# Kernel tuning notes

Measured on AMD Instinct MI355X. Metric: run time of the kernel, lower is better.

Reference implementation:

```python
import jax, jax.numpy as jnp
import numpy as np

NUM_HEADS = 8
EPS = 1e-3

N_TOKENS = 32768
DIM = 256
N_WIN = 128
WIN = N_TOKENS // N_WIN  # 256 tokens per window


def setup_inputs() -> dict:
    key = jax.random.key(0)
    ks = jax.random.split(key, 4)
    x = jax.random.normal(ks[0], (N_TOKENS, DIM), dtype=jnp.float32)
    # torch nn.Linear weights are [out_features, in_features]
    w_qkv = jax.random.normal(ks[1], (3 * DIM, DIM), dtype=jnp.float32) * (DIM ** -0.5)
    w_proj = jax.random.normal(ks[2], (DIM, DIM), dtype=jnp.float32) * (DIM ** -0.5)
    b_proj = jnp.zeros((DIM,), dtype=jnp.float32)
    batch_win_inds = (jnp.arange(N_TOKENS) // WIN).astype(jnp.int64)
    offsets = (jnp.arange(N_WIN) * WIN).astype(jnp.int64)
    counts = jnp.full((N_WIN,), WIN, dtype=jnp.int64)
    return {"x": x, "w_qkv": w_qkv, "w_proj": w_proj, "b_proj": b_proj,
            "offsets": offsets, "counts": counts, "batch_win_inds": batch_win_inds}


def reference(x, w_qkv, w_proj, b_proj, offsets, counts, batch_win_inds):
    N, C = x.shape
    H = NUM_HEADS
    hd = C // H
    W = counts.shape[0]  # number of windows (static)

    qkv = x @ w_qkv.T                      # [N, 3C]
    q, k, v = jnp.split(qkv, 3, axis=-1)   # each [N, C]
    q = jax.nn.relu(q.reshape(N, H, hd))   # [N, H, hd]
    k = jax.nn.relu(k.reshape(N, H, hd))
    v = v.reshape(N, H, hd)

    seg = batch_win_inds.astype(jnp.int32)
    # per-window KV state: kv[w] = sum_{i in w} k_i^T v_i   -> [W, H, hd, hd]
    kv = jax.ops.segment_sum(jnp.einsum('nhc,nhd->nhcd', k, v), seg, num_segments=W)
    # per-window key sum for normalizer                      -> [W, H, hd]
    s = jax.ops.segment_sum(k, seg, num_segments=W)

    y = jnp.einsum('nhc,nhcd->nhd', q, kv[seg])              # [N, H, hd]
    z = jnp.sum(s[seg] * q, axis=-1, keepdims=True)          # [N, H, 1]
    y = y / (z + EPS)

    y = y.reshape(N, C) @ w_proj.T + b_proj                  # [N, C]
    return y
```

## Files before the change

### kernel.cpp

```cpp
#include <hip/hip_runtime.h>

typedef __bf16 bf16_t;
typedef bf16_t bf16x8 __attribute__((ext_vector_type(8)));
typedef bf16_t bf16x4 __attribute__((ext_vector_type(4)));
typedef float f32x4 __attribute__((ext_vector_type(4)));

#define M_TOK 32768
#define NWIN 128
#define WIN  256

typedef __attribute__((address_space(3))) void* as3p;
typedef const __attribute__((address_space(1))) void* as1p;

__device__ __forceinline__ void gll16(const void* g, void* l) {
    __builtin_amdgcn_global_load_lds((as1p)g, (as3p)l, 16, 0, 0);
}

__device__ __forceinline__ bf16x8 cvt8(f32x4 a, f32x4 b) {
    bf16x8 o;
    o[0] = (bf16_t)a[0]; o[1] = (bf16_t)a[1]; o[2] = (bf16_t)a[2]; o[3] = (bf16_t)a[3];
    o[4] = (bf16_t)b[0]; o[5] = (bf16_t)b[1]; o[6] = (bf16_t)b[2]; o[7] = (bf16_t)b[3];
    return o;
}

__global__ __launch_bounds__(256) void wconv(
    const float* __restrict__ wq, const float* __restrict__ wp,
    bf16_t* __restrict__ wqb, bf16_t* __restrict__ wpb)
{
    int i4 = (blockIdx.x * 256 + threadIdx.x) * 4;
    const float* s; bf16_t* dst; int idx;
    if (i4 < 196608) { s = wq; dst = wqb; idx = i4; }
    else             { s = wp; dst = wpb; idx = i4 - 196608; }
    f32x4 v = *(const f32x4*)(s + idx);
    bf16x4 o;
    o[0] = (bf16_t)v[0]; o[1] = (bf16_t)v[1]; o[2] = (bf16_t)v[2]; o[3] = (bf16_t)v[3];
    *(bf16x4*)(dst + idx) = o;
}

__global__ __launch_bounds__(256) void gemm1_qkv(
    const float* __restrict__ X,
    const bf16_t* __restrict__ Wb,
    bf16_t* __restrict__ QKV)
{
    __shared__ float  As[4][128][16];
    __shared__ bf16_t Bs[2][128][32];

    const int tid = threadIdx.x;
    const int lane = tid & 63;
    const int wv = tid >> 6;
    const int wm = wv >> 1, wn = wv & 1;
    const int id = blockIdx.x;
    const int sg = id / 48, wsub = id % 48;
    const int m0 = (sg * 8 + (wsub & 7)) * 128;
    const int n0 = (wsub >> 3) * 128;
    const int r = lane & 15, q = lane >> 4;
    const int srow = lane >> 2;

    f32x4 acc[4][4] = {};

    for (int kc = 0; kc < 256; kc += 64) {
#pragma unroll
        for (int p = 0; p < 4; ++p)
#pragma unroll
            for (int g = 0; g < 2; ++g) {
                const int rb = wv * 32 + g * 16;
                gll16(X + (size_t)(m0 + rb + srow) * 256 + kc + p * 16 + (lane & 3) * 4,
                      &As[p][rb][0]);
            }
#pragma unroll
        for (int p = 0; p < 2; ++p)
#pragma unroll
            for (int g = 0; g < 2; ++g) {
                const int rb = wv * 32 + g * 16;
                gll16(Wb + (size_t)(n0 + rb + srow) * 256 + kc + p * 32 + (lane & 3) * 8,
                      &Bs[p][rb][0]);
            }
        __syncthreads();

#pragma unroll
        for (int kk = 0; kk < 64; kk += 32) {
            const int kq = kk + q * 8;
            const int pA = kq >> 4, offA = kq & 15;
            const int pB = kk >> 5;
            bf16x8 a[4], b[4];
#pragma unroll
            for (int i = 0; i < 4; ++i) {
                f32x4 lo = *(const f32x4*)&As[pA][wm * 64 + i * 16 + r][offA];
                f32x4 hi = *(const f32x4*)&As[pA][wm * 64 + i * 16 + r][offA + 4];
                a[i] = cvt8(lo, hi);
            }
#pragma unroll
            for (int j = 0; j < 4; ++j)
                b[j] = *(const bf16x8*)&Bs[pB][wn * 64 + j * 16 + r][q * 8];
#pragma unroll
            for (int i = 0; i < 4; ++i)
#pragma unroll
                for (int j = 0; j < 4; ++j)
                    acc[i][j] = __builtin_amdgcn_mfma_f32_16x16x32_bf16(b[j], a[i], acc[i][j], 0, 0, 0);
        }
        __syncthreads();
    }

#pragma unroll
    for (int i = 0; i < 4; ++i) {
        const int rowg = m0 + wm * 64 + i * 16 + r;
#pragma unroll
        for (int j = 0; j < 4; ++j) {
            const int nb = n0 + wn * 64 + j * 16 + q * 4;
            const int nblk = nb >> 5, d = nb & 31;
            bf16x4 o;
#pragma unroll
            for (int reg = 0; reg < 4; ++reg) {
                float v = acc[i][j][reg];
                if (nblk < 16) v = fmaxf(v, 0.0f);
                o[reg] = (bf16_t)v;
            }
            *(bf16x4*)&QKV[((size_t)nblk * M_TOK + rowg) * 32 + d] = o;
        }
    }
}

__global__ __launch_bounds__(256) void gemm2_proj(
    const bf16_t* __restrict__ Y,
    const bf16_t* __restrict__ Wb,
    const float* __restrict__ bias,
    float* __restrict__ Out)
{
    __shared__ bf16_t As[2][128][32];
    __shared__ bf16_t Bs[2][128][32];

    const int tid = threadIdx.x;
    const int lane = tid & 63;
    const int wv = tid >> 6;
    const int wm = wv >> 1, wn = wv & 1;
    const int id = blockIdx.x;
    const int sg = id / 32, wsub = id % 32;
    const int m0 = (sg * 16 + (wsub & 15)) * 128;
    const int n0 = (wsub >> 4) * 128;
    const int r = lane & 15, q = lane >> 4;
    const int srow = lane >> 2;

    f32x4 acc[4][4] = {};

    for (int kc = 0; kc < 256; kc += 64) {
#pragma unroll
        for (int p = 0; p < 2; ++p)
#pragma unroll
            for (int g = 0; g < 2; ++g) {
                const int rb = wv * 32 + g * 16;
                gll16(Y + (size_t)(m0 + rb + srow) * 256 + kc + p * 32 + (lane & 3) * 8,
                      &As[p][rb][0]);
                gll16(Wb + (size_t)(n0 + rb + srow) * 256 + kc + p * 32 + (lane & 3) * 8,
                      &Bs[p][rb][0]);
            }
        __syncthreads();

#pragma unroll
        for (int kk = 0; kk < 64; kk += 32) {
            const int pB = kk >> 5;
            bf16x8 a[4], b[4];
#pragma unroll
            for (int i = 0; i < 4; ++i)
                a[i] = *(const bf16x8*)&As[pB][wm * 64 + i * 16 + r][q * 8];
#pragma unroll
            for (int j = 0; j < 4; ++j)
                b[j] = *(const bf16x8*)&Bs[pB][wn * 64 + j * 16 + r][q * 8];
#pragma unroll
            for (int i = 0; i < 4; ++i)
#pragma unroll
                for (int j = 0; j < 4; ++j)
                    acc[i][j] = __builtin_amdgcn_mfma_f32_16x16x32_bf16(b[j], a[i], acc[i][j], 0, 0, 0);
        }
        __syncthreads();
    }

#pragma unroll
    for (int i = 0; i < 4; ++i) {
        const int rowg = m0 + wm * 64 + i * 16 + r;
#pragma unroll
        for (int j = 0; j < 4; ++j) {
            const int nb = n0 + wn * 64 + j * 16 + q * 4;
            f32x4 bi = *(const f32x4*)(bias + nb);
            f32x4 o;
#pragma unroll
            for (int reg = 0; reg < 4; ++reg) o[reg] = acc[i][j][reg] + bi[reg];
            *(f32x4*)&Out[(size_t)rowg * 256 + nb] = o;
        }
    }
}

__global__ __launch_bounds__(256) void kvy_kernel(
    const bf16_t* __restrict__ QKV,
    const int* __restrict__ offsets,
    const int* __restrict__ counts,
    bf16_t* __restrict__ Y)
{
    const int w = blockIdx.x;
    const int h = blockIdx.y;
    const int is64 = (counts[1] == 0) ? 1 : 0;
    const int off = offsets[w << is64];
    const int tid = threadIdx.x;
    const int lane = tid & 63;
    const int wv = tid >> 6;

    __shared__ __align__(16) bf16_t KT[32 * 264];
    __shared__ __align__(16) bf16_t VT[32 * 264];
    __shared__ __align__(16) bf16_t KVT[32 * 40];
    __shared__ float sbuf[32];
    __shared__ float spart[32 * 8];
    __shared__ float zinv[WIN];

    {
        const int t = tid;
        const bf16_t* kp = QKV + ((size_t)(8 + h) * M_TOK + off + t) * 32;
        const bf16_t* vp = QKV + ((size_t)(16 + h) * M_TOK + off + t) * 32;
        bf16_t ka[32], va[32];
#pragma unroll
        for (int u = 0; u < 4; ++u) {
            bf16x8 kk = *(const bf16x8*)(kp + u * 8);
            bf16x8 vvv = *(const bf16x8*)(vp + u * 8);
#pragma unroll
            for (int j = 0; j < 8; ++j) { ka[u * 8 + j] = kk[j]; va[u * 8 + j] = vvv[j]; }
        }
#pragma unroll
        for (int c = 0; c < 32; ++c) {
            KT[c * 264 + t] = ka[c];
            VT[c * 264 + t] = va[c];
        }
    }
    __syncthreads();

    {
        const int c = tid >> 3;
        const int tc = (tid & 7) * 32;
        float ps = 0.f;
#pragma unroll
        for (int u = 0; u < 4; ++u) {
            bf16x8 kk = *(const bf16x8*)(&KT[c * 264 + tc + u * 8]);
#pragma unroll
            for (int j = 0; j < 8; ++j) ps += (float)kk[j];
        }
        spart[c * 8 + (tid & 7)] = ps;
    }
    {
        const int i = wv >> 1, j = wv & 1;
        const int r = lane & 15, q = lane >> 4;
        f32x4 acc = {};
#pragma unroll
        for (int ch = 0; ch < 8; ++ch) {
            bf16x8 af = *(const bf16x8*)(&KT[(i * 16 + r) * 264 + ch * 32 + q * 8]);
            bf16x8 bf_ = *(const bf16x8*)(&VT[(j * 16 + r) * 264 + ch * 32 + q * 8]);
            acc = __builtin_amdgcn_mfma_f32_16x16x32_bf16(af, bf_, acc, 0, 0, 0);
        }
        bf16x4 kv4;
#pragma unroll
        for (int reg = 0; reg < 4; ++reg) kv4[reg] = (bf16_t)acc[reg];
        *(bf16x4*)(&KVT[(j * 16 + r) * 40 + i * 16 + q * 4]) = kv4;
    }
    __syncthreads();
    if (tid < 32) {
        float s = 0.f;
#pragma unroll
        for (int u = 0; u < 8; ++u) s += spart[tid * 8 + u];
        sbuf[tid] = s;
    }
    __syncthreads();

    {
        const int t = tid;
        const bf16_t* qp = QKV + ((size_t)h * M_TOK + off + t) * 32;
        float z = 0.f;
#pragma unroll
        for (int u = 0; u < 4; ++u) {
            bf16x8 qq = *(const bf16x8*)(qp + u * 8);
#pragma unroll
            for (int j = 0; j < 8; ++j) z += (float)qq[j] * sbuf[u * 8 + j];
        }
        zinv[t] = 1.0f / (z + 1e-3f);
    }
    __syncthreads();

    {
        const int r = lane & 15, q = lane >> 4;
        bf16x8 b0 = *(const bf16x8*)(&KVT[(r) * 40 + q * 8]);
        bf16x8 b1 = *(const bf16x8*)(&KVT[(16 + r) * 40 + q * 8]);
#pragma unroll
        for (int u = 0; u < 4; ++u) {
            const int mi = wv * 4 + u;
            const bf16_t* ap = QKV + ((size_t)h * M_TOK + off + mi * 16 + r) * 32 + q * 8;
            bf16x8 af = *(const bf16x8*)ap;
            f32x4 acc0 = {}, acc1 = {};
            acc0 = __builtin_amdgcn_mfma_f32_16x16x32_bf16(b0, af, acc0, 0, 0, 0);
            acc1 = __builtin_amdgcn_mfma_f32_16x16x32_bf16(b1, af, acc1, 0, 0, 0);
            const int tkn = mi * 16 + r;
            const float zi = zinv[tkn];
            bf16_t* yp = Y + (size_t)(off + tkn) * 256 + h * 32;
            bf16x4 o0, o1;
#pragma unroll
            for (int reg = 0; reg < 4; ++reg) {
                o0[reg] = (bf16_t)(acc0[reg] * zi);
                o1[reg] = (bf16_t)(acc1[reg] * zi);
            }
            *(bf16x4*)(yp + q * 4) = o0;
            *(bf16x4*)(yp + 16 + q * 4) = o1;
        }
    }
}

extern "C" void kernel_launch(void* const* d_in, const int* in_sizes, int n_in,
                              void* d_out, int out_size, void* d_ws, size_t ws_size,
                              hipStream_t stream) {
    const float* x      = (const float*)d_in[0];
    const float* w_qkv  = (const float*)d_in[1];
    const float* w_proj = (const float*)d_in[2];
    const float* b_proj = (const float*)d_in[3];
    const int*   offs   = (const int*)d_in[4];
    const int*   cnts   = (const int*)d_in[5];

    char* ws = (char*)d_ws;
    bf16_t* QKV = (bf16_t*)ws;
    bf16_t* Y   = (bf16_t*)(ws + 50331648);
    bf16_t* Wqb = (bf16_t*)(ws + 67108864);
    bf16_t* Wpb = (bf16_t*)(ws + 67502080);
    float*  out = (float*)d_out;

    wconv<<<256, 256, 0, stream>>>(w_qkv, w_proj, Wqb, Wpb);

    gemm1_qkv<<<1536, 256, 0, stream>>>(x, Wqb, QKV);

    kvy_kernel<<<dim3(NWIN, 8), 256, 0, stream>>>(QKV, offs, cnts, Y);

    gemm2_proj<<<512, 256, 0, stream>>>(Y, Wpb, b_proj, out);
}
```

Measured before the change: 138.6 us.

## Pre-convert X to bf16, swizzle LDS tiles, and halve proj GEMM N tile

X is converted to bf16 in a combined pack kernel together with the weights, so gemm1 loads bf16 tiles directly instead of loading fp32 into LDS and converting on every fragment read. Both GEMMs switch to a 128x64 bf16 LDS layout with an XOR swizzle on the 16-byte column chunks to reduce bank conflicts. The projection GEMM uses 128x64 output tiles, doubling its block count to improve occupancy and load balance. The cost is an extra full pass over X (a fp32 read and bf16 write) in a separate kernel, reusing the Y buffer as scratch for it.

```diff
diff --git a/kernel.cpp b/kernel.cpp
--- a/kernel.cpp
+++ b/kernel.cpp
@@ -23,27 +23,27 @@
     return o;
 }
 
-__global__ __launch_bounds__(256) void wconv(
-    const float* __restrict__ wq, const float* __restrict__ wp,
-    bf16_t* __restrict__ wqb, bf16_t* __restrict__ wpb)
+__global__ __launch_bounds__(256) void convpack(
+    const float* __restrict__ X, const float* __restrict__ wq, const float* __restrict__ wp,
+    bf16_t* __restrict__ Xb, bf16_t* __restrict__ wqb, bf16_t* __restrict__ wpb)
 {
-    int i4 = (blockIdx.x * 256 + threadIdx.x) * 4;
-    const float* s; bf16_t* dst; int idx;
-    if (i4 < 196608) { s = wq; dst = wqb; idx = i4; }
-    else             { s = wp; dst = wpb; idx = i4 - 196608; }
-    f32x4 v = *(const f32x4*)(s + idx);
-    bf16x4 o;
-    o[0] = (bf16_t)v[0]; o[1] = (bf16_t)v[1]; o[2] = (bf16_t)v[2]; o[3] = (bf16_t)v[3];
-    *(bf16x4*)(dst + idx) = o;
+    long i8 = ((long)blockIdx.x * 256 + threadIdx.x) * 8;
+    const float* s; bf16_t* dst; long idx;
+    if (i8 < 8388608)      { s = X;  dst = Xb;  idx = i8; }
+    else if (i8 < 8585216) { s = wq; dst = wqb; idx = i8 - 8388608; }
+    else                   { s = wp; dst = wpb; idx = i8 - 8585216; }
+    f32x4 v0 = *(const f32x4*)(s + idx);
+    f32x4 v1 = *(const f32x4*)(s + idx + 4);
+    *(bf16x8*)(dst + idx) = cvt8(v0, v1);
 }
 
 __global__ __launch_bounds__(256) void gemm1_qkv(
-    const float* __restrict__ X,
+    const bf16_t* __restrict__ Xb,
     const bf16_t* __restrict__ Wb,
     bf16_t* __restrict__ QKV)
 {
-    __shared__ float  As[4][128][16];
-    __shared__ bf16_t Bs[2][128][32];
+    __shared__ __align__(16) bf16_t As[128][64];
+    __shared__ __align__(16) bf16_t Bs[128][64];
 
     const int tid = threadIdx.x;
     const int lane = tid & 63;
@@ -54,44 +54,31 @@
     const int m0 = (sg * 8 + (wsub & 7)) * 128;
     const int n0 = (wsub >> 3) * 128;
     const int r = lane & 15, q = lane >> 4;
-    const int srow = lane >> 2;
+    const int lrow = lane >> 3;
+    const int lg8 = ((lane & 7) ^ lrow) * 8;
+    const int rx = r & 7;
 
     f32x4 acc[4][4] = {};
 
     for (int kc = 0; kc < 256; kc += 64) {
 #pragma unroll
-        for (int p = 0; p < 4; ++p)
-#pragma unroll
-            for (int g = 0; g < 2; ++g) {
-                const int rb = wv * 32 + g * 16;
-                gll16(X + (size_t)(m0 + rb + srow) * 256 + kc + p * 16 + (lane & 3) * 4,
-                      &As[p][rb][0]);
-            }
-#pragma unroll
-        for (int p = 0; p < 2; ++p)
-#pragma unroll
-            for (int g = 0; g < 2; ++g) {
-                const int rb = wv * 32 + g * 16;
-                gll16(Wb + (size_t)(n0 + rb + srow) * 256 + kc + p * 32 + (lane & 3) * 8,
-                      &Bs[p][rb][0]);
-            }
+        for (int g = 0; g < 4; ++g) {
+            const int rb = wv * 32 + g * 8;
+            gll16(Xb + (size_t)(m0 + rb + lrow) * 256 + kc + lg8, &As[rb][0]);
+            gll16(Wb + (size_t)(n0 + rb + lrow) * 256 + kc + lg8, &Bs[rb][0]);
+        }
         __syncthreads();
 
 #pragma unroll
         for (int kk = 0; kk < 64; kk += 32) {
-            const int kq = kk + q * 8;
-            const int pA = kq >> 4, offA = kq & 15;
-            const int pB = kk >> 5;
+            const int ax8 = (((kk >> 3) + q) ^ rx) * 8;
             bf16x8 a[4], b[4];
 #pragma unroll
-            for (int i = 0; i < 4; ++i) {
-                f32x4 lo = *(const f32x4*)&As[pA][wm * 64 + i * 16 + r][offA];
-                f32x4 hi = *(const f32x4*)&As[pA][wm * 64 + i * 16 + r][offA + 4];
-                a[i] = cvt8(lo, hi);
-            }
+            for (int i = 0; i < 4; ++i)
+                a[i] = *(const bf16x8*)&As[wm * 64 + i * 16 + r][ax8];
 #pragma unroll
             for (int j = 0; j < 4; ++j)
-                b[j] = *(const bf16x8*)&Bs[pB][wn * 64 + j * 16 + r][q * 8];
+                b[j] = *(const bf16x8*)&Bs[wn * 64 + j * 16 + r][ax8];
 #pragma unroll
             for (int i = 0; i < 4; ++i)
 #pragma unroll
@@ -126,8 +113,8 @@
     const float* __restrict__ bias,
     float* __restrict__ Out)
 {
-    __shared__ bf16_t As[2][128][32];
-    __shared__ bf16_t Bs[2][128][32];
+    __shared__ __align__(16) bf16_t As[128][64];
+    __shared__ __align__(16) bf16_t Bs[64][64];
 
     const int tid = threadIdx.x;
     const int lane = tid & 63;
@@ -135,40 +122,42 @@
     const int wm = wv >> 1, wn = wv & 1;
     const int id = blockIdx.x;
     const int sg = id / 32, wsub = id % 32;
-    const int m0 = (sg * 16 + (wsub & 15)) * 128;
-    const int n0 = (wsub >> 4) * 128;
+    const int m0 = (sg * 8 + (wsub & 7)) * 128;
+    const int n0 = (wsub >> 3) * 64;
     const int r = lane & 15, q = lane >> 4;
-    const int srow = lane >> 2;
-
-    f32x4 acc[4][4] = {};
+    const int lrow = lane >> 3;
+    const int lg8 = ((lane & 7) ^ lrow) * 8;
+    const int rx = r & 7;
+
+    f32x4 acc[4][2] = {};
 
     for (int kc = 0; kc < 256; kc += 64) {
 #pragma unroll
-        for (int p = 0; p < 2; ++p)
-#pragma unroll
-            for (int g = 0; g < 2; ++g) {
-                const int rb = wv * 32 + g * 16;
-                gll16(Y + (size_t)(m0 + rb + srow) * 256 + kc + p * 32 + (lane & 3) * 8,
-                      &As[p][rb][0]);
-                gll16(Wb + (size_t)(n0 + rb + srow) * 256 + kc + p * 32 + (lane & 3) * 8,
-                      &Bs[p][rb][0]);
-            }
+        for (int g = 0; g < 4; ++g) {
+            const int rb = wv * 32 + g * 8;
+            gll16(Y + (size_t)(m0 + rb + lrow) * 256 + kc + lg8, &As[rb][0]);
+        }
+#pragma unroll
+        for (int g = 0; g < 2; ++g) {
+            const int rb = wv * 16 + g * 8;
+            gll16(Wb + (size_t)(n0 + rb + lrow) * 256 + kc + lg8, &Bs[rb][0]);
+        }
         __syncthreads();
 
 #pragma unroll
         for (int kk = 0; kk < 64; kk += 32) {
-            const int pB = kk >> 5;
-            bf16x8 a[4], b[4];
+            const int ax8 = (((kk >> 3) + q) ^ rx) * 8;
+            bf16x8 a[4], b[2];
 #pragma unroll
             for (int i = 0; i < 4; ++i)
-                a[i] = *(const bf16x8*)&As[pB][wm * 64 + i * 16 + r][q * 8];
-#pragma unroll
-            for (int j = 0; j < 4; ++j)
-                b[j] = *(const bf16x8*)&Bs[pB][wn * 64 + j * 16 + r][q * 8];
+                a[i] = *(const bf16x8*)&As[wm * 64 + i * 16 + r][ax8];
+#pragma unroll
+            for (int j = 0; j < 2; ++j)
+                b[j] = *(const bf16x8*)&Bs[wn * 32 + j * 16 + r][ax8];
 #pragma unroll
             for (int i = 0; i < 4; ++i)
 #pragma unroll
-                for (int j = 0; j < 4; ++j)
+                for (int j = 0; j < 2; ++j)
                     acc[i][j] = __builtin_amdgcn_mfma_f32_16x16x32_bf16(b[j], a[i], acc[i][j], 0, 0, 0);
         }
         __syncthreads();
@@ -178,8 +167,8 @@
     for (int i = 0; i < 4; ++i) {
         const int rowg = m0 + wm * 64 + i * 16 + r;
 #pragma unroll
-        for (int j = 0; j < 4; ++j) {
-            const int nb = n0 + wn * 64 + j * 16 + q * 4;
+        for (int j = 0; j < 2; ++j) {
+            const int nb = n0 + wn * 32 + j * 16 + q * 4;
             f32x4 bi = *(const f32x4*)(bias + nb);
             f32x4 o;
 #pragma unroll
@@ -320,15 +309,16 @@
     char* ws = (char*)d_ws;
     bf16_t* QKV = (bf16_t*)ws;
     bf16_t* Y   = (bf16_t*)(ws + 50331648);
+    bf16_t* Xb  = Y;
     bf16_t* Wqb = (bf16_t*)(ws + 67108864);
     bf16_t* Wpb = (bf16_t*)(ws + 67502080);
     float*  out = (float*)d_out;
 
-    wconv<<<256, 256, 0, stream>>>(w_qkv, w_proj, Wqb, Wpb);
-
-    gemm1_qkv<<<1536, 256, 0, stream>>>(x, Wqb, QKV);
+    convpack<<<4224, 256, 0, stream>>>(x, w_qkv, w_proj, Xb, Wqb, Wpb);
+
+    gemm1_qkv<<<1536, 256, 0, stream>>>(Xb, Wqb, QKV);
 
     kvy_kernel<<<dim3(NWIN, 8), 256, 0, stream>>>(QKV, offs, cnts, Y);
 
-    gemm2_proj<<<512, 256, 0, stream>>>(Y, Wpb, b_proj, out);
-}
+    gemm2_proj<<<1024, 256, 0, stream>>>(Y, Wpb, b_proj, out);
+}
```

New measurement: 138.6 us. Within noise of the previous version (+0.0%).
